# Kernel optimization log

Hardware: AMD Instinct MI355X
Metric: run time of the kernel (lower is better)

Reference implementation:

```python
import jax, jax.numpy as jnp
import numpy as np

B, T, D, H = 4, 2048, 1024, 4
DK = D // H      # head_k_dim = 256
DV = D // H      # head_v_dim = 256
M = DK           # num_slots defaults to head_k_dim
GATE_NORM = 16.0
CLAMP_MIN, CLAMP_MAX = -32.0, 32.0
EPS = 1e-5
ROPE_BASE = 10000.0


def setup_inputs() -> dict:
    key = jax.random.key(0)
    ks = jax.random.split(key, 8)
    sd = 0.02  # stands in for xavier_uniform with gain 2**-2.5
    return {
        "hidden_states": jax.random.normal(ks[0], (B, T, D), jnp.float32),
        "q_w": jax.random.normal(ks[1], (D, D), jnp.float32) * sd,
        "k_w": jax.random.normal(ks[2], (D, D), jnp.float32) * sd,
        "v_w": jax.random.normal(ks[3], (D, D), jnp.float32) * sd,
        "g_w": jax.random.normal(ks[4], (D, D), jnp.float32) * sd,
        "s_w": jax.random.normal(ks[5], (D, H * M), jnp.float32) * sd,
        "sg_w": jax.random.normal(ks[6], (D, H), jnp.float32) * sd,
        "gn_w": jnp.ones((DV,), jnp.float32),
        "o_w": jax.random.normal(ks[7], (D, D), jnp.float32) * sd,
    }


def _rope(x):
    # x: [B, T, H, DK]; non-interleaved (flash-attn style) rotary, full head dim
    half = x.shape[-1] // 2
    inv = 1.0 / (ROPE_BASE ** (jnp.arange(half, dtype=jnp.float32) / half))
    ang = jnp.arange(x.shape[1], dtype=jnp.float32)[:, None] * inv[None, :]  # [T, half]
    cos = jnp.cos(ang)[None, :, None, :]
    sin = jnp.sin(ang)[None, :, None, :]
    x1, x2 = x[..., :half], x[..., half:]
    return jnp.concatenate([x1 * cos - x2 * sin, x2 * cos + x1 * sin], -1)


def _abc(q, k, v, s):
    # ABC linear attention with slot memory (fla chunk_abc semantics, g=None path).
    # q, k: [B,H,T,DK]; v: [B,H,T,DV]; s: [B,H,T,M] (clamped slot logits)
    scale = q.shape[-1] ** -0.5
    z = jax.lax.cumlogsumexp(s, axis=2)                    # running log-normalizer
    s_n = jnp.exp(s - z)                                   # normalized slot write weights
    g = jnp.exp(jnp.concatenate([z[:, :, :1], z[:, :, :-1]], 2) - z)  # per-step decay in (0,1]

    tm = lambda x: jnp.moveaxis(x, 2, 0)                   # time-major for scan

    # stage 1: key memory  hk[B,H,DK,M];  ok_t = scale * q_t @ hk_t
    def step_k(hk, inp):
        q_t, k_t, s_t, g_t = inp
        hk = hk * g_t[:, :, None, :] + k_t[..., None] * s_t[:, :, None, :]
        return hk, jnp.einsum('bhk,bhkm->bhm', q_t, hk)
    hk0 = jnp.zeros(q.shape[:2] + (q.shape[-1], s.shape[-1]), q.dtype)
    _, ok = jax.lax.scan(step_k, hk0, (tm(q * scale), tm(k), tm(s_n), tm(g)))

    qv = jax.nn.softmax(ok, axis=-1)                       # slot read weights, [T,B,H,M]

    # stage 2: value memory  hv[B,H,M,DV];  ov_t = qv_t @ hv_t
    def step_v(hv, inp):
        qv_t, v_t, s_t, g_t = inp
        hv = hv * g_t[..., None] + s_t[..., None] * v_t[:, :, None, :]
        return hv, jnp.einsum('bhm,bhmv->bhv', qv_t, hv)
    hv0 = jnp.zeros(v.shape[:2] + (s.shape[-1], v.shape[-1]), v.dtype)
    _, ov = jax.lax.scan(step_v, hv0, (qv, tm(v), tm(s_n), tm(g)))
    return jnp.moveaxis(ov, 0, 2)                          # [B,H,T,DV]


def reference(hidden_states, q_w, k_w, v_w, g_w, s_w, sg_w, gn_w, o_w):
    x = hidden_states
    q = (x @ q_w).reshape(B, T, H, DK)
    k = (x @ k_w).reshape(B, T, H, DK)
    v = (x @ v_w).reshape(B, T, H, DV).transpose(0, 2, 1, 3)       # [B,H,T,DV]
    q, k = _rope(q), _rope(k)
    q = q.transpose(0, 2, 1, 3)                                    # [B,H,T,DK]
    k = k.transpose(0, 2, 1, 3)

    s = (x @ s_w).reshape(B, T, H, M).transpose(0, 2, 1, 3)        # [B,H,T,M]
    s = jnp.clip(s, CLAMP_MIN, CLAMP_MAX)

    sg = jax.nn.log_sigmoid(x @ sg_w).transpose(0, 2, 1) / GATE_NORM  # [B,H,T]
    k = k * jnp.exp(jnp.cumsum(sg, axis=2))[..., None]

    o = _abc(q, k, v, s).transpose(0, 2, 1, 3)                     # [B,T,H,DV]

    g = (x @ g_w).reshape(B, T, H, DV)
    rms = o * jax.lax.rsqrt(jnp.mean(o * o, axis=-1, keepdims=True) + EPS) * gn_w
    o = (rms * g * jax.nn.sigmoid(g)).reshape(B, T, D)             # RMSNorm + swish gate
    return o @ o_w
```

## Files before the change

kernel.cpp:

```cpp
#include <hip/hip_runtime.h>
#include <hip/hip_bf16.h>
#include <stdint.h>
#include <stddef.h>
#include <math.h>

typedef __bf16 bf8_t __attribute__((ext_vector_type(8)));
typedef __bf16 bf4_t __attribute__((ext_vector_type(4)));
typedef float  f4_t  __attribute__((ext_vector_type(4)));
typedef unsigned int u32;

#define DEV static __device__ __forceinline__

namespace abc {
constexpr int B = 4, T = 2048, D = 1024, H = 4;
constexpr int BT = B * T;
constexpr int CH = 64;
constexpr int NC = T / CH;
constexpr int BH = B * H;
constexpr float SCALE = 0.0625f;
constexpr float GN = 16.0f;
constexpr float EPS = 1e-5f;
}

DEV f4_t mfma16(bf8_t a, bf8_t b, f4_t c) {
  return __builtin_amdgcn_mfma_f32_16x16x32_bf16(a, b, c, 0, 0, 0);
}

DEV void glds16(const void* g, void* l) {
  __builtin_amdgcn_global_load_lds(
      (const __attribute__((address_space(1))) u32*)g,
      (__attribute__((address_space(3))) u32*)l, 16, 0, 0);
}

DEV __bf16* slice_addr(__bf16* base, int row, int cg ) {
  return base + (((cg >> 2) * 2 + (row >> 7)) * 4096
               + ((((row & 127) << 2) | ((cg & 3) ^ (row & 3))) * 8));
}
DEV const __bf16* slice_addr(const __bf16* base, int row, int cg) {
  return base + (((cg >> 2) * 2 + (row >> 7)) * 4096
               + ((((row & 127) << 2) | ((cg & 3) ^ (row & 3))) * 8));
}

DEV void stage_lin(const __bf16* __restrict__ g, __bf16* lds, int tid) {
  #pragma unroll
  for (int i = 0; i < 2; i++)
    glds16(g + (size_t)(i * 256 + tid) * 8, lds + (i * 256 + (tid & ~63)) * 8);
}

template<int ROWS>
DEV void stage(const __bf16* __restrict__ g, int S ,
               __bf16* lds, int tid) {
  #pragma unroll
  for (int i = 0; i < ROWS / 64; i++) {
    int p = i * 256 + tid;
    int m = p >> 2;
    int q = (p & 3) ^ (m & 3);
    glds16(g + (size_t)m * S + q * 8, lds + (i * 256 + (tid & ~63)) * 8);
  }
}
DEV bf8_t bfrag(const __bf16* sl, int m, int quad) {
  return *reinterpret_cast<const bf8_t*>(sl + m * 32 + ((quad ^ (m & 3)) << 3));
}

DEV void ring_pre(int s) {
  if (s < 46)       asm volatile("s_waitcnt vmcnt(4)" ::: "memory");
  else if (s == 46) asm volatile("s_waitcnt vmcnt(2)" ::: "memory");
  else              asm volatile("s_waitcnt vmcnt(0)" ::: "memory");
  asm volatile("s_waitcnt lgkmcnt(0)" ::: "memory");
  asm volatile("s_barrier" ::: "memory");
}

DEV void stage_g(const __bf16* __restrict__ g, int S, __bf16* lds, int tid) {
  int m = tid >> 2;
  int q = (tid & 3) ^ ((m >> 1) & 3);
  glds16(g + (size_t)m * S + q * 8, lds + (tid & ~63) * 8);
}
DEV bf8_t bfrag_g(const __bf16* sl, int m, int quad) {
  return *reinterpret_cast<const bf8_t*>(sl + m * 32 + (((quad ^ (m >> 1)) & 3) << 3));
}

__global__ __launch_bounds__(256)
void cvt_x_kernel(const float* __restrict__ x, __bf16* __restrict__ xb)
{
  const int idx = blockIdx.x * 256 + threadIdx.x;
  const float4* src = reinterpret_cast<const float4*>(x);
  float4 a = src[(size_t)idx * 2];
  float4 b = src[(size_t)idx * 2 + 1];
  bf8_t o;
  o[0] = (__bf16)a.x; o[1] = (__bf16)a.y; o[2] = (__bf16)a.z; o[3] = (__bf16)a.w;
  o[4] = (__bf16)b.x; o[5] = (__bf16)b.y; o[6] = (__bf16)b.z; o[7] = (__bf16)b.w;
  reinterpret_cast<bf8_t*>(xb)[idx] = o;
}

__global__ __launch_bounds__(256)
void cvt_w_kernel(const float* __restrict__ w0, const float* __restrict__ w1,
                  const float* __restrict__ w2, const float* __restrict__ w3,
                  const float* __restrict__ w4, const float* __restrict__ w5,
                  __bf16* __restrict__ wt)
{
  const int z = blockIdx.z;
  const float* W = (z == 0) ? w0 : (z == 1) ? w1 : (z == 2) ? w2
                 : (z == 3) ? w3 : (z == 4) ? w4 : w5;
  const int n0 = blockIdx.x * 64, k0 = blockIdx.y * 64;
  __shared__ __bf16 Ts[64][72];
  const int tid = threadIdx.x;
  #pragma unroll
  for (int i = 0; i < 4; i++) {
    int p = tid + 256 * i;
    int row = p >> 4, c4 = p & 15;
    float4 v = *reinterpret_cast<const float4*>(W + (size_t)(k0 + row) * 1024 + n0 + c4 * 4);
    Ts[c4 * 4 + 0][row] = (__bf16)v.x;
    Ts[c4 * 4 + 1][row] = (__bf16)v.y;
    Ts[c4 * 4 + 2][row] = (__bf16)v.z;
    Ts[c4 * 4 + 3][row] = (__bf16)v.w;
  }
  __syncthreads();
  #pragma unroll
  for (int i = 0; i < 2; i++) {
    int p = tid + 256 * i;
    int n = p >> 3, kq = p & 7;
    bf8_t o = *reinterpret_cast<const bf8_t*>(&Ts[n][kq * 8]);
    *reinterpret_cast<bf8_t*>(wt + (size_t)z * 1024 * 1024 + (size_t)(n0 + n) * 1024 + k0 + kq * 8) = o;
  }
}

template<bool OUT_BF16, int NZ>
__global__ __launch_bounds__(512, 2)
void gemm256_kernel(const __bf16* __restrict__ A, const __bf16* __restrict__ BtB,
                    void* __restrict__ Cp)
{
  using namespace abc;
  constexpr int K = 1024;
  constexpr int NZT = 4 * NZ;
  const int bflat = blockIdx.x;
  const int xcd = bflat & 7;
  const int j = bflat >> 3;
  const int m_local = j / NZT;
  const int nz = j % NZT;
  const int nt = nz & 3, z = nz >> 2;
  const int m0 = (xcd * 4 + m_local) * 256;
  const int n0 = nt * 256;
  const __bf16* Bt = BtB + (size_t)z * K * 1024;

  __shared__ __bf16 LA[2][4][4096];
  __shared__ __bf16 LB[2][4][4096];

  const int tid = threadIdx.x;
  const int lane = tid & 63, wv = tid >> 6;
  const int wr = wv >> 2, wc = wv & 3;
  const int quad = lane >> 4, l16 = lane & 15;
  const f4_t fzero = {0.f, 0.f, 0.f, 0.f};
  f4_t acc[8][4];
  #pragma unroll
  for (int fr = 0; fr < 8; fr++)
    #pragma unroll
    for (int fc = 0; fc < 4; fc++) acc[fr][fc] = fzero;

  auto issue4 = [&](int kt, int ks) {
    const int db = kt & 1;
    const int kcol = kt * 64 + ks * 32;
    stage_g(A  + (size_t)(m0 +   0) * K + kcol, K, &LA[db][0 + ks][0], tid);
    stage_g(A  + (size_t)(m0 + 128) * K + kcol, K, &LA[db][2 + ks][0], tid);
    stage_g(Bt + (size_t)(n0 +   0) * K + kcol, K, &LB[db][0 + ks][0], tid);
    stage_g(Bt + (size_t)(n0 + 128) * K + kcol, K, &LB[db][2 + ks][0], tid);
  };

  issue4(0, 0); issue4(0, 1);

  for (int kt = 0; kt < 16; kt++) {
    const int db = kt & 1;
    const bool last = (kt == 15);
    #pragma unroll
    for (int ks = 0; ks < 2; ks++) {
      if (last && ks == 1) asm volatile("s_waitcnt vmcnt(0)\ns_barrier" ::: "memory");
      else                 asm volatile("s_waitcnt vmcnt(4)\ns_barrier" ::: "memory");
      bf8_t af[8], bfv[4];
      #pragma unroll
      for (int fr = 0; fr < 8; fr++)
        af[fr] = bfrag_g(&LA[db][wr * 2 + ks][0], fr * 16 + l16, quad);
      #pragma unroll
      for (int fc = 0; fc < 4; fc++)
        bfv[fc] = bfrag_g(&LB[db][(wc >> 1) * 2 + ks][0], (wc & 1) * 64 + fc * 16 + l16, quad);
      if (!last) issue4(kt + 1, ks);
      __builtin_amdgcn_s_setprio(1);
      #pragma unroll
      for (int fr = 0; fr < 8; fr++)
        #pragma unroll
        for (int fc = 0; fc < 4; fc++)
          acc[fr][fc] = mfma16(af[fr], bfv[fc], acc[fr][fc]);
      __builtin_amdgcn_s_setprio(0);
    }
  }

  const int crow = m0 + wr * 128, ccol = n0 + wc * 64;
  if (OUT_BF16) {
    __bf16* C = (__bf16*)Cp + (size_t)z * BT * 1024;
    #pragma unroll
    for (int fr = 0; fr < 8; fr++)
      #pragma unroll
      for (int fc = 0; fc < 4; fc++)
        #pragma unroll
        for (int r = 0; r < 4; r++)
          C[(size_t)(crow + fr * 16 + quad * 4 + r) * 1024 + ccol + fc * 16 + l16] =
              (__bf16)acc[fr][fc][r];
  } else {
    float* C = (float*)Cp;
    #pragma unroll
    for (int fr = 0; fr < 8; fr++)
      #pragma unroll
      for (int fc = 0; fc < 4; fc++)
        #pragma unroll
        for (int r = 0; r < 4; r++)
          C[(size_t)(crow + fr * 16 + quad * 4 + r) * 1024 + ccol + fc * 16 + l16] =
              acc[fr][fc][r];
  }
}

__global__ __launch_bounds__(256)
void sg_kernel(const float* __restrict__ x, const float* __restrict__ sgw,
               float* __restrict__ sgl)
{
  using namespace abc;
  const int wvid = threadIdx.x >> 6, lane = threadIdx.x & 63;
  const int bt = blockIdx.x * 4 + wvid;
  const float* xr = x + (size_t)bt * 1024;
  float a0 = 0, a1 = 0, a2 = 0, a3 = 0;
  #pragma unroll 4
  for (int u = 0; u < 16; u++) {
    int i = u * 64 + lane;
    float xv = xr[i];
    float4 w = *reinterpret_cast<const float4*>(sgw + (size_t)i * 4);
    a0 += xv * w.x; a1 += xv * w.y; a2 += xv * w.z; a3 += xv * w.w;
  }
  #pragma unroll
  for (int off = 32; off > 0; off >>= 1) {
    a0 += __shfl_down(a0, off);
    a1 += __shfl_down(a1, off);
    a2 += __shfl_down(a2, off);
    a3 += __shfl_down(a3, off);
  }
  if (lane == 0) {
    const int b = bt >> 11, t = bt & (T - 1);
    float r[4] = {a0, a1, a2, a3};
    #pragma unroll
    for (int h = 0; h < 4; h++) {
      float v = r[h];
      float ls = fminf(v, 0.f) - log1pf(expf(-fabsf(v)));
      sgl[(size_t)(b * 4 + h) * T + t] = ls * (1.0f / GN);
    }
  }
}

__global__ __launch_bounds__(256)
void scan_kernel(const float* __restrict__ sgl, float* __restrict__ sgc)
{
  using namespace abc;
  const int bh = blockIdx.x;
  const float* in = sgl + (size_t)bh * T;
  float* out = sgc + (size_t)bh * T;
  __shared__ float part[256];
  const int tid = threadIdx.x;
  float v[8]; float s = 0.f;
  #pragma unroll
  for (int i = 0; i < 8; i++) { v[i] = in[tid * 8 + i]; s += v[i]; }
  part[tid] = s;
  __syncthreads();
  for (int off = 1; off < 256; off <<= 1) {
    float a = (tid >= off) ? part[tid - off] : 0.f;
    __syncthreads();
    part[tid] += a;
    __syncthreads();
  }
  float run = (tid > 0) ? part[tid - 1] : 0.f;
  #pragma unroll
  for (int i = 0; i < 8; i++) { run += v[i]; out[tid * 8 + i] = run; }
}

__global__ __launch_bounds__(256)
void prep_kernel(__bf16* __restrict__ q, __bf16* __restrict__ k,
                 __bf16* __restrict__ s, const float* __restrict__ sgc)
{
  using namespace abc;
  const int bt = blockIdx.x;
  const int b = bt >> 11, t = bt & (T - 1);
  const int tid = threadIdx.x;
  const size_t ro = (size_t)bt * 1024;
  #pragma unroll
  for (int i = 0; i < 2; i++) {
    int p = tid + 256 * i;
    int h = p >> 7, d = p & 127;
    float inv = expf(-(float)d * (9.210340371976184f / 128.0f));
    float ang = (float)t * inv;
    float sn, cs;
    sincosf(ang, &sn, &cs);
    size_t base = ro + (size_t)h * 256 + d;
    float q1 = (float)q[base], q2 = (float)q[base + 128];
    q[base]       = (__bf16)(q1 * cs - q2 * sn);
    q[base + 128] = (__bf16)(q2 * cs + q1 * sn);
    float dec = expf(sgc[(size_t)(b * 4 + h) * T + t]);
    float k1 = (float)k[base], k2 = (float)k[base + 128];
    k[base]       = (__bf16)((k1 * cs - k2 * sn) * dec);
    k[base + 128] = (__bf16)((k2 * cs + k1 * sn) * dec);
  }
  #pragma unroll
  for (int i = 0; i < 4; i++) {
    int e = tid + 256 * i;
    float v = (float)s[ro + e];
    v = fminf(fmaxf(v, -32.f), 32.f);
    s[ro + e] = (__bf16)expf(v);
  }
}

template<bool NEW0, bool NEW1>
__global__ __launch_bounds__(256)
void transpose_kernel(const __bf16* __restrict__ s0, const __bf16* __restrict__ s1,
                      __bf16* __restrict__ d0, __bf16* __restrict__ d1)
{
  using namespace abc;
  const int c = blockIdx.x, bh = blockIdx.y, z = blockIdx.z;
  const int b = bh >> 2, h = bh & 3;
  const size_t R = (size_t)b * T + (size_t)c * CH;
  const int F = h * 256;
  const __bf16* src = z ? s1 : s0;
  __bf16* dst = (z ? d1 : d0) + ((size_t)bh * NC + c) * (256 * 64);
  const bool NEWL = z ? NEW1 : NEW0;
  __shared__ __bf16 L[256 * 64];
  const int tid = threadIdx.x;
  #pragma unroll
  for (int j = 0; j < 8; j++) {
    int p = tid + 256 * j;
    int t = p >> 5, fc = p & 31;
    bf8_t v = *reinterpret_cast<const bf8_t*>(src + (R + t) * 1024 + F + fc * 8);
    const int sw = ((t >> 3) ^ (fc & 7)) * 8 + (t & 7);
    #pragma unroll
    for (int u = 0; u < 8; u++)
      L[(fc * 8 + u) * 64 + sw] = v[u];
  }
  __syncthreads();
  #pragma unroll
  for (int j = 0; j < 8; j++) {
    int p = tid + 256 * j;
    int f = p >> 3, q = p & 7;
    int phys = q ^ ((f >> 3) & 7);
    bf8_t o = *reinterpret_cast<const bf8_t*>(&L[f * 64 + phys * 8]);
    __bf16* daddr = NEWL ? slice_addr(dst, f, q)
                         : dst + (size_t)f * 64 + q * 8;
    *reinterpret_cast<bf8_t*>(daddr) = o;
  }
}

__global__ __launch_bounds__(256)
void chunkstate_kernel(const __bf16* __restrict__ KT, const __bf16* __restrict__ VT,
                       const __bf16* __restrict__ AT,
                       __bf16* __restrict__ HKc, __bf16* __restrict__ HVc,
                       float* __restrict__ csA)
{
  using namespace abc;
  const int c = blockIdx.x, bh = blockIdx.y, part = blockIdx.z;
  const size_t TB = ((size_t)bh * NC + c) * (256 * 64);
  const bool isHV = part >= 2;
  const int p2 = part & 1;
  const __bf16* Aop = (isHV ? VT : AT) + TB;
  const __bf16* Bop = (isHV ? AT : KT) + TB;
  const int tid = threadIdx.x;
  if (part == 2) {
    float ssum = 0.f;
    #pragma unroll
    for (int u = 0; u < 8; u++) {
      bf8_t v = *reinterpret_cast<const bf8_t*>(slice_addr(AT + TB, tid, u));
      #pragma unroll
      for (int w = 0; w < 8; w++) ssum += (float)v[w];
    }
    csA[((size_t)bh * NC + c) * 256 + tid] = ssum;
  }
  const int lane = tid & 63, wvid = tid >> 6;
  const int quad = lane >> 4, l16 = lane & 15;
  const int row0 = p2 * 128 + wvid * 32;
  const f4_t fzero = {0.f, 0.f, 0.f, 0.f};
  f4_t acc[2][16];
  #pragma unroll
  for (int a = 0; a < 2; a++)
    #pragma unroll
    for (int ct = 0; ct < 16; ct++) acc[a][ct] = fzero;
  #pragma unroll
  for (int ks = 0; ks < 2; ks++) {
    const int cg = ks * 4 + quad;
    bf8_t af0 = *reinterpret_cast<const bf8_t*>(slice_addr(Aop, row0 + l16, cg));
    bf8_t af1 = *reinterpret_cast<const bf8_t*>(slice_addr(Aop, row0 + 16 + l16, cg));
    #pragma unroll
    for (int ct = 0; ct < 16; ct++) {
      bf8_t bv;
      if (isHV)
        bv = *reinterpret_cast<const bf8_t*>(slice_addr(Bop, ct * 16 + l16, cg));
      else
        bv = *reinterpret_cast<const bf8_t*>(Bop + (size_t)(ct * 16 + l16) * 64 + ks * 32 + quad * 8);
      acc[0][ct] = mfma16(af0, bv, acc[0][ct]);
      acc[1][ct] = mfma16(af1, bv, acc[1][ct]);
    }
  }
  __bf16* out = (isHV ? HVc : HKc) + ((size_t)bh * NC + c) * 65536;
  #pragma unroll
  for (int rt = 0; rt < 2; rt++)
    #pragma unroll
    for (int ct = 0; ct < 16; ct++)
      #pragma unroll
      for (int r = 0; r < 4; r++) {
        const int mg = row0 + rt * 16 + quad * 4 + r;
        const int n  = ct * 16 + l16;
        *(slice_addr(out, mg, n >> 3) + (n & 7)) = (__bf16)acc[rt][ct][r];
      }
}

__global__ __launch_bounds__(256)
void prefix_state_kernel(__bf16* __restrict__ HKc, __bf16* __restrict__ HVc)
{
  using namespace abc;
  const int bh = blockIdx.y;
  __bf16* base = (blockIdx.z ? HVc : HKc) + (size_t)bh * NC * 65536;
  const int e = (blockIdx.x * 256 + threadIdx.x) * 8;
  float run[8];
  #pragma unroll
  for (int u = 0; u < 8; u++) run[u] = 0.f;
  #pragma unroll 4
  for (int c = 0; c < NC; c++) {
    __bf16* p = base + (size_t)c * 65536 + e;
    bf8_t v = *reinterpret_cast<const bf8_t*>(p);
    bf8_t o;
    #pragma unroll
    for (int u = 0; u < 8; u++) { o[u] = (__bf16)run[u]; run[u] += (float)v[u]; }
    *reinterpret_cast<bf8_t*>(p) = o;
  }
}

__global__ __launch_bounds__(256)
void prefix_csa_kernel(float* __restrict__ csA)
{
  using namespace abc;
  const int bh = blockIdx.x, m = threadIdx.x;
  float run = 0.f;
  for (int c = 0; c < NC; c++) {
    float* p = csA + ((size_t)bh * NC + c) * 256 + m;
    float v = *p; *p = run; run += v;
  }
}

__global__ __launch_bounds__(256)
void attn_kernel(const __bf16* __restrict__ qg, const __bf16* __restrict__ kg,
                 const __bf16* __restrict__ ag, const __bf16* __restrict__ gg,
                 const __bf16* __restrict__ ATp, const __bf16* __restrict__ VTp,
                 const __bf16* __restrict__ HKp, const __bf16* __restrict__ HVp,
                 const float* __restrict__ Zp, const float* __restrict__ gnw,
                 __bf16* __restrict__ yout)
{
  using namespace abc;
  const int c = blockIdx.x, bh = blockIdx.y;
  const int b = bh >> 2, h = bh & 3;
  const size_t R = (size_t)b * T + (size_t)c * CH;
  const int F = h * 256;
  const int tid = threadIdx.x;
  const int lane = tid & 63, wvid = tid >> 6;
  const int quad = lane >> 4, l16 = lane & 15;

  __shared__ __bf16 ST[4][4096];
  __shared__ __bf16 Ws[64][264];
  __shared__ __bf16 S1s[64][72];
  __shared__ float zs[256];
  __shared__ float gns[256];

  const __bf16* atb = ATp + ((size_t)bh * NC + c) * (256 * 64);
  const __bf16* vtb = VTp + ((size_t)bh * NC + c) * (256 * 64);
  const __bf16* hkb = HKp + ((size_t)bh * NC + c) * 65536;
  const __bf16* hvb = HVp + ((size_t)bh * NC + c) * 65536;
  const __bf16* kbase = kg + R * 1024 + F;
  const __bf16* abase = ag + R * 1024 + F;

  zs[tid] = Zp[((size_t)bh * NC + c) * 256 + tid];
  gns[tid] = gnw[tid];
  __syncthreads();

  const __bf16* qrow = qg + (R + wvid * 16 + l16) * 1024 + F;
  bf8_t aq[8];
  #pragma unroll
  for (int ks = 0; ks < 8; ks++)
    aq[ks] = *reinterpret_cast<const bf8_t*>(qrow + ks * 32 + quad * 8);

  const f4_t fzero = {0.f, 0.f, 0.f, 0.f};

  auto issue = [&](int s) {
    if (s >= 48) return;
    __bf16* buf = &ST[s & 3][0];
    if (s < 4) {
      stage<64>(kbase + (2 * s) * 32, 1024, buf, tid);
      stage<64>(kbase + (2 * s + 1) * 32, 1024, buf + 2048, tid);
    } else if (s < 8) {
      stage_lin(atb + (s - 4) * 4096, buf, tid);
    } else if (s < 24) {
      stage_lin(hkb + (s - 8) * 4096, buf, tid);
    } else if (s < 28) {
      int j = s - 24;
      stage<64>(abase + (2 * j) * 32, 1024, buf, tid);
      stage<64>(abase + (2 * j + 1) * 32, 1024, buf + 2048, tid);
    } else if (s < 44) {
      stage_lin(hvb + (s - 28) * 4096, buf, tid);
    } else {
      stage_lin(vtb + (s - 44) * 4096, buf, tid);
    }
  };

  issue(0); issue(1); issue(2);

  f4_t s1a[4];
  #pragma unroll
  for (int it = 0; it < 4; it++) s1a[it] = fzero;
  #pragma unroll
  for (int j = 0; j < 4; j++) {
    ring_pre(j);
    issue(j + 3);
    const __bf16* sl = &ST[j & 3][0];
    #pragma unroll
    for (int ks2 = 0; ks2 < 2; ks2++) {
      bf8_t a = aq[2 * j + ks2];
      const __bf16* sb = sl + ks2 * 2048;
      #pragma unroll
      for (int it = 0; it < 4; it++)
        s1a[it] = mfma16(a, bfrag(sb, it * 16 + l16, quad), s1a[it]);
    }
  }
  #pragma unroll
  for (int it = 0; it < 4; it++)
    #pragma unroll
    for (int r = 0; r < 4; r++) {
      int tl = wvid * 16 + quad * 4 + r;
      int il = it * 16 + l16;
      S1s[tl][il] = (il <= tl) ? (__bf16)s1a[it][r] : (__bf16)0.0f;
    }

  f4_t aok[16], acum[16];
  #pragma unroll
  for (int mt = 0; mt < 16; mt++) { aok[mt] = fzero; acum[mt] = fzero; }
  #pragma unroll
  for (int j = 0; j < 4; j++) {
    int s = 4 + j, iks = j >> 1, rh = j & 1;
    ring_pre(s);
    issue(s + 3);
    const __bf16* sl = &ST[s & 3][0];
    bf8_t s1f = *reinterpret_cast<const bf8_t*>(&S1s[wvid * 16 + l16][iks * 32 + quad * 8]);
    bf8_t lf;
    #pragma unroll
    for (int u = 0; u < 8; u++)
      lf[u] = (iks * 32 + quad * 8 + u <= wvid * 16 + l16) ? (__bf16)1.0f : (__bf16)0.0f;
    #pragma unroll
    for (int m8 = 0; m8 < 8; m8++) {
      bf8_t bfa = bfrag(sl, m8 * 16 + l16, quad);
      aok[rh * 8 + m8]  = mfma16(s1f, bfa, aok[rh * 8 + m8]);
      acum[rh * 8 + m8] = mfma16(lf,  bfa, acum[rh * 8 + m8]);
    }
  }

  #pragma unroll
  for (int j = 0; j < 16; j++) {
    int s = 8 + j, ks = j >> 1, rh = j & 1;
    ring_pre(s);
    issue(s + 3);
    const __bf16* sl = &ST[s & 3][0];
    #pragma unroll
    for (int m8 = 0; m8 < 8; m8++) {
      bf8_t bv = bfrag(sl, m8 * 16 + l16, quad);
      aok[rh * 8 + m8] = mfma16(aq[ks], bv, aok[rh * 8 + m8]);
    }
  }

  #pragma unroll
  for (int r = 0; r < 4; r++) {
    float ovv[16], sa[16];
    float mx = -3.0e38f;
    #pragma unroll
    for (int mt = 0; mt < 16; mt++) {
      sa[mt] = zs[mt * 16 + l16] + acum[mt][r];
      ovv[mt] = SCALE * aok[mt][r] / sa[mt];
      mx = fmaxf(mx, ovv[mt]);
    }
    #pragma unroll
    for (int off = 1; off < 16; off <<= 1) mx = fmaxf(mx, __shfl_xor(mx, off));
    float se = 0.f;
    #pragma unroll
    for (int mt = 0; mt < 16; mt++) { ovv[mt] = __expf(ovv[mt] - mx); se += ovv[mt]; }
    #pragma unroll
    for (int off = 1; off < 16; off <<= 1) se += __shfl_xor(se, off);
    float inv = 1.0f / se;
    int tl = wvid * 16 + quad * 4 + r;
    #pragma unroll
    for (int mt = 0; mt < 16; mt++)
      Ws[tl][mt * 16 + l16] = (__bf16)(ovv[mt] * inv / sa[mt]);
  }

  f4_t pacc[4];
  #pragma unroll
  for (int it = 0; it < 4; it++) pacc[it] = fzero;
  #pragma unroll
  for (int j = 0; j < 4; j++) {
    int s = 24 + j;
    ring_pre(s);
    issue(s + 3);
    const __bf16* sl = &ST[s & 3][0];
    #pragma unroll
    for (int ks2 = 0; ks2 < 2; ks2++) {
      int ks = 2 * j + ks2;
      bf8_t wf = *reinterpret_cast<const bf8_t*>(&Ws[wvid * 16 + l16][ks * 32 + quad * 8]);
      const __bf16* sb = sl + ks2 * 2048;
      #pragma unroll
      for (int it = 0; it < 4; it++)
        pacc[it] = mfma16(wf, bfrag(sb, it * 16 + l16, quad), pacc[it]);
    }
  }
  #pragma unroll
  for (int it = 0; it < 4; it++)
    #pragma unroll
    for (int r = 0; r < 4; r++) {
      int tl = wvid * 16 + quad * 4 + r;
      int il = it * 16 + l16;
      S1s[tl][il] = (il <= tl) ? (__bf16)pacc[it][r] : (__bf16)0.0f;
    }

  f4_t oacc[16];
  #pragma unroll
  for (int vt = 0; vt < 16; vt++) oacc[vt] = fzero;
  #pragma unroll
  for (int j = 0; j < 16; j++) {
    int s = 28 + j, ks = j >> 1, rh = j & 1;
    ring_pre(s);
    issue(s + 3);
    const __bf16* sl = &ST[s & 3][0];
    bf8_t wf = *reinterpret_cast<const bf8_t*>(&Ws[wvid * 16 + l16][ks * 32 + quad * 8]);
    #pragma unroll
    for (int v8 = 0; v8 < 8; v8++) {
      bf8_t bv = bfrag(sl, v8 * 16 + l16, quad);
      oacc[rh * 8 + v8] = mfma16(wf, bv, oacc[rh * 8 + v8]);
    }
  }

  #pragma unroll
  for (int j = 0; j < 4; j++) {
    int s = 44 + j, iks = j >> 1, rh = j & 1;
    ring_pre(s);
    issue(s + 3);
    const __bf16* sl = &ST[s & 3][0];
    bf8_t pf = *reinterpret_cast<const bf8_t*>(&S1s[wvid * 16 + l16][iks * 32 + quad * 8]);
    #pragma unroll
    for (int v8 = 0; v8 < 8; v8++) {
      bf8_t bvt = bfrag(sl, v8 * 16 + l16, quad);
      oacc[rh * 8 + v8] = mfma16(pf, bvt, oacc[rh * 8 + v8]);
    }
  }

  #pragma unroll
  for (int r = 0; r < 4; r++) {
    float ss = 0.f;
    #pragma unroll
    for (int vt = 0; vt < 16; vt++) ss += oacc[vt][r] * oacc[vt][r];
    #pragma unroll
    for (int off = 1; off < 16; off <<= 1) ss += __shfl_xor(ss, off);
    float rinv = rsqrtf(ss * (1.0f / 256.0f) + EPS);
    int tl = wvid * 16 + quad * 4 + r;
    const __bf16* grow = gg + (R + tl) * 1024 + F;
    __bf16* yrow = yout + (R + tl) * 1024 + F;
    #pragma unroll
    for (int vt = 0; vt < 16; vt++) {
      int v = vt * 16 + l16;
      float gvl = (float)grow[v];
      float yv = oacc[vt][r] * rinv * gns[v] * gvl / (1.0f + __expf(-gvl));
      yrow[v] = (__bf16)yv;
    }
  }
}

extern "C" void kernel_launch(void* const* d_in, const int* in_sizes, int n_in,
                              void* d_out, int out_size, void* d_ws, size_t ws_size,
                              hipStream_t stream) {
  using namespace abc;
  (void)in_sizes; (void)n_in; (void)out_size; (void)ws_size;
  const float* x    = (const float*)d_in[0];
  const float* q_w  = (const float*)d_in[1];
  const float* k_w  = (const float*)d_in[2];
  const float* v_w  = (const float*)d_in[3];
  const float* g_w  = (const float*)d_in[4];
  const float* s_w  = (const float*)d_in[5];
  const float* sg_w = (const float*)d_in[6];
  const float* gn_w = (const float*)d_in[7];
  const float* o_w  = (const float*)d_in[8];
  float* out = (float*)d_out;

  char* ws = (char*)d_ws;
  const size_t PROJ = (size_t)BT * 1024;
  __bf16* proj = (__bf16*)ws;
  __bf16* q_bf = proj + 0 * PROJ;
  __bf16* k_bf = proj + 1 * PROJ;
  __bf16* v_bf = proj + 2 * PROJ;
  __bf16* g_bf = proj + 3 * PROJ;
  __bf16* a_bf = proj + 4 * PROJ;
  __bf16* xb   = proj + 5 * PROJ;
  float* sgl = (float*)(ws + (size_t)96 * 1024 * 1024);
  float* sgc = sgl + (size_t)BH * T;
  float* csA = sgc + (size_t)BH * T;
  __bf16* HKc = (__bf16*)(ws + (size_t)97 * 1024 * 1024);
  __bf16* HVc = HKc + (size_t)BH * NC * 65536;
  __bf16* wt  = (__bf16*)(ws + (size_t)225 * 1024 * 1024);
  __bf16* KT  = (__bf16*)(ws + (size_t)237 * 1024 * 1024);
  __bf16* VT  = xb;
  __bf16* AT  = v_bf;
  __bf16* y_bf = KT;

  dim3 blk(256);
  dim3 blk512(512);
  cvt_w_kernel<<<dim3(16, 16, 6), blk, 0, stream>>>(q_w, k_w, v_w, g_w, s_w, o_w, wt);
  cvt_x_kernel<<<dim3(BT * 1024 / (256 * 8)), blk, 0, stream>>>(x, xb);
  gemm256_kernel<true, 5><<<dim3(32 * 4 * 5), blk512, 0, stream>>>(xb, wt, proj);
  sg_kernel<<<dim3(BT / 4), blk, 0, stream>>>(x, sg_w, sgl);
  scan_kernel<<<dim3(BH), blk, 0, stream>>>(sgl, sgc);
  prep_kernel<<<dim3(BT), blk, 0, stream>>>(q_bf, k_bf, a_bf, sgc);
  transpose_kernel<false, true><<<dim3(NC, BH, 2), blk, 0, stream>>>(k_bf, v_bf, KT, VT);
  transpose_kernel<true, true><<<dim3(NC, BH, 1), blk, 0, stream>>>(a_bf, a_bf, AT, AT);
  chunkstate_kernel<<<dim3(NC, BH, 4), blk, 0, stream>>>(KT, VT, AT, HKc, HVc, csA);
  prefix_state_kernel<<<dim3(32, BH, 2), blk, 0, stream>>>(HKc, HVc);
  prefix_csa_kernel<<<dim3(BH), blk, 0, stream>>>(csA);
  attn_kernel<<<dim3(NC, BH), blk, 0, stream>>>(
      q_bf, k_bf, a_bf, g_bf, AT, VT, HKc, HVc, csA, gn_w, y_bf);
  gemm256_kernel<false, 1><<<dim3(32 * 4), blk512, 0, stream>>>(
      y_bf, wt + (size_t)5 * 1024 * 1024, out);
}
```

Baseline: 515.9 us.

## Load attention operands directly from global memory instead of LDS ring pipeline

Removes the 4-slot LDS staging ring, with its async global-to-LDS copies, waitcnt and barrier calls, from the attention kernel. MFMA B-fragments for K, A, AT, HK, HV and VT now come straight from global memory into registers, using the precomputed swizzled layout offsets. This drops the per-stage barriers and frees 32KB of LDS, which may raise occupancy. In exchange, each of the four waves now fetches the same operand data separately from global/L2, and the explicit prefetch overlap is lost.

Result: faster. 473.9 us (-8.2%).

```diff
diff --git a/kernel.cpp b/kernel.cpp
--- a/kernel.cpp
+++ b/kernel.cpp
@@ -5,7 +5,6 @@
 #include <math.h>
 
 typedef __bf16 bf8_t __attribute__((ext_vector_type(8)));
-typedef __bf16 bf4_t __attribute__((ext_vector_type(4)));
 typedef float  f4_t  __attribute__((ext_vector_type(4)));
 typedef unsigned int u32;
 
@@ -39,35 +38,6 @@
 DEV const __bf16* slice_addr(const __bf16* base, int row, int cg) {
   return base + (((cg >> 2) * 2 + (row >> 7)) * 4096
                + ((((row & 127) << 2) | ((cg & 3) ^ (row & 3))) * 8));
-}
-
-DEV void stage_lin(const __bf16* __restrict__ g, __bf16* lds, int tid) {
-  #pragma unroll
-  for (int i = 0; i < 2; i++)
-    glds16(g + (size_t)(i * 256 + tid) * 8, lds + (i * 256 + (tid & ~63)) * 8);
-}
-
-template<int ROWS>
-DEV void stage(const __bf16* __restrict__ g, int S ,
-               __bf16* lds, int tid) {
-  #pragma unroll
-  for (int i = 0; i < ROWS / 64; i++) {
-    int p = i * 256 + tid;
-    int m = p >> 2;
-    int q = (p & 3) ^ (m & 3);
-    glds16(g + (size_t)m * S + q * 8, lds + (i * 256 + (tid & ~63)) * 8);
-  }
-}
-DEV bf8_t bfrag(const __bf16* sl, int m, int quad) {
-  return *reinterpret_cast<const bf8_t*>(sl + m * 32 + ((quad ^ (m & 3)) << 3));
-}
-
-DEV void ring_pre(int s) {
-  if (s < 46)       asm volatile("s_waitcnt vmcnt(4)" ::: "memory");
-  else if (s == 46) asm volatile("s_waitcnt vmcnt(2)" ::: "memory");
-  else              asm volatile("s_waitcnt vmcnt(0)" ::: "memory");
-  asm volatile("s_waitcnt lgkmcnt(0)" ::: "memory");
-  asm volatile("s_barrier" ::: "memory");
 }
 
 DEV void stage_g(const __bf16* __restrict__ g, int S, __bf16* lds, int tid) {
@@ -461,7 +431,6 @@
   const int lane = tid & 63, wvid = tid >> 6;
   const int quad = lane >> 4, l16 = lane & 15;
 
-  __shared__ __bf16 ST[4][4096];
   __shared__ __bf16 Ws[64][264];
   __shared__ __bf16 S1s[64][72];
   __shared__ float zs[256];
@@ -478,6 +447,9 @@
   gns[tid] = gnw[tid];
   __syncthreads();
 
+  const int lsw = l16 * 32 + ((quad ^ (l16 & 3)) << 3);
+  const int rowoff = l16 * 1024 + quad * 8;
+
   const __bf16* qrow = qg + (R + wvid * 16 + l16) * 1024 + F;
   bf8_t aq[8];
   #pragma unroll
@@ -486,44 +458,15 @@
 
   const f4_t fzero = {0.f, 0.f, 0.f, 0.f};
 
-  auto issue = [&](int s) {
-    if (s >= 48) return;
-    __bf16* buf = &ST[s & 3][0];
-    if (s < 4) {
-      stage<64>(kbase + (2 * s) * 32, 1024, buf, tid);
-      stage<64>(kbase + (2 * s + 1) * 32, 1024, buf + 2048, tid);
-    } else if (s < 8) {
-      stage_lin(atb + (s - 4) * 4096, buf, tid);
-    } else if (s < 24) {
-      stage_lin(hkb + (s - 8) * 4096, buf, tid);
-    } else if (s < 28) {
-      int j = s - 24;
-      stage<64>(abase + (2 * j) * 32, 1024, buf, tid);
-      stage<64>(abase + (2 * j + 1) * 32, 1024, buf + 2048, tid);
-    } else if (s < 44) {
-      stage_lin(hvb + (s - 28) * 4096, buf, tid);
-    } else {
-      stage_lin(vtb + (s - 44) * 4096, buf, tid);
-    }
-  };
-
-  issue(0); issue(1); issue(2);
-
   f4_t s1a[4];
   #pragma unroll
   for (int it = 0; it < 4; it++) s1a[it] = fzero;
   #pragma unroll
-  for (int j = 0; j < 4; j++) {
-    ring_pre(j);
-    issue(j + 3);
-    const __bf16* sl = &ST[j & 3][0];
-    #pragma unroll
-    for (int ks2 = 0; ks2 < 2; ks2++) {
-      bf8_t a = aq[2 * j + ks2];
-      const __bf16* sb = sl + ks2 * 2048;
-      #pragma unroll
-      for (int it = 0; it < 4; it++)
-        s1a[it] = mfma16(a, bfrag(sb, it * 16 + l16, quad), s1a[it]);
+  for (int ks = 0; ks < 8; ks++) {
+    #pragma unroll
+    for (int it = 0; it < 4; it++) {
+      bf8_t bk = *reinterpret_cast<const bf8_t*>(kbase + it * 16 * 1024 + rowoff + ks * 32);
+      s1a[it] = mfma16(aq[ks], bk, s1a[it]);
     }
   }
   #pragma unroll
@@ -539,34 +482,32 @@
   #pragma unroll
   for (int mt = 0; mt < 16; mt++) { aok[mt] = fzero; acum[mt] = fzero; }
   #pragma unroll
-  for (int j = 0; j < 4; j++) {
-    int s = 4 + j, iks = j >> 1, rh = j & 1;
-    ring_pre(s);
-    issue(s + 3);
-    const __bf16* sl = &ST[s & 3][0];
+  for (int iks = 0; iks < 2; iks++) {
     bf8_t s1f = *reinterpret_cast<const bf8_t*>(&S1s[wvid * 16 + l16][iks * 32 + quad * 8]);
     bf8_t lf;
     #pragma unroll
     for (int u = 0; u < 8; u++)
       lf[u] = (iks * 32 + quad * 8 + u <= wvid * 16 + l16) ? (__bf16)1.0f : (__bf16)0.0f;
     #pragma unroll
-    for (int m8 = 0; m8 < 8; m8++) {
-      bf8_t bfa = bfrag(sl, m8 * 16 + l16, quad);
-      aok[rh * 8 + m8]  = mfma16(s1f, bfa, aok[rh * 8 + m8]);
-      acum[rh * 8 + m8] = mfma16(lf,  bfa, acum[rh * 8 + m8]);
-    }
-  }
-
-  #pragma unroll
-  for (int j = 0; j < 16; j++) {
-    int s = 8 + j, ks = j >> 1, rh = j & 1;
-    ring_pre(s);
-    issue(s + 3);
-    const __bf16* sl = &ST[s & 3][0];
-    #pragma unroll
-    for (int m8 = 0; m8 < 8; m8++) {
-      bf8_t bv = bfrag(sl, m8 * 16 + l16, quad);
-      aok[rh * 8 + m8] = mfma16(aq[ks], bv, aok[rh * 8 + m8]);
+    for (int rh = 0; rh < 2; rh++) {
+      #pragma unroll
+      for (int m8 = 0; m8 < 8; m8++) {
+        bf8_t bfa = *reinterpret_cast<const bf8_t*>(atb + (iks * 2 + rh) * 4096 + m8 * 512 + lsw);
+        aok[rh * 8 + m8]  = mfma16(s1f, bfa, aok[rh * 8 + m8]);
+        acum[rh * 8 + m8] = mfma16(lf,  bfa, acum[rh * 8 + m8]);
+      }
+    }
+  }
+
+  #pragma unroll
+  for (int ks = 0; ks < 8; ks++) {
+    #pragma unroll
+    for (int rh = 0; rh < 2; rh++) {
+      #pragma unroll
+      for (int m8 = 0; m8 < 8; m8++) {
+        bf8_t bv = *reinterpret_cast<const bf8_t*>(hkb + (ks * 2 + rh) * 4096 + m8 * 512 + lsw);
+        aok[rh * 8 + m8] = mfma16(aq[ks], bv, aok[rh * 8 + m8]);
+      }
     }
   }
 
@@ -598,19 +539,12 @@
   #pragma unroll
   for (int it = 0; it < 4; it++) pacc[it] = fzero;
   #pragma unroll
-  for (int j = 0; j < 4; j++) {
-    int s = 24 + j;
-    ring_pre(s);
-    issue(s + 3);
-    const __bf16* sl = &ST[s & 3][0];
-    #pragma unroll
-    for (int ks2 = 0; ks2 < 2; ks2++) {
-      int ks = 2 * j + ks2;
-      bf8_t wf = *reinterpret_cast<const bf8_t*>(&Ws[wvid * 16 + l16][ks * 32 + quad * 8]);
-      const __bf16* sb = sl + ks2 * 2048;
-      #pragma unroll
-      for (int it = 0; it < 4; it++)
-        pacc[it] = mfma16(wf, bfrag(sb, it * 16 + l16, quad), pacc[it]);
+  for (int ks = 0; ks < 8; ks++) {
+    bf8_t wf = *reinterpret_cast<const bf8_t*>(&Ws[wvid * 16 + l16][ks * 32 + quad * 8]);
+    #pragma unroll
+    for (int it = 0; it < 4; it++) {
+      bf8_t ba = *reinterpret_cast<const bf8_t*>(abase + it * 16 * 1024 + rowoff + ks * 32);
+      pacc[it] = mfma16(wf, ba, pacc[it]);
     }
   }
   #pragma unroll
@@ -626,30 +560,28 @@
   #pragma unroll
   for (int vt = 0; vt < 16; vt++) oacc[vt] = fzero;
   #pragma unroll
-  for (int j = 0; j < 16; j++) {
-    int s = 28 + j, ks = j >> 1, rh = j & 1;
-    ring_pre(s);
-    issue(s + 3);
-    const __bf16* sl = &ST[s & 3][0];
+  for (int ks = 0; ks < 8; ks++) {
     bf8_t wf = *reinterpret_cast<const bf8_t*>(&Ws[wvid * 16 + l16][ks * 32 + quad * 8]);
     #pragma unroll
-    for (int v8 = 0; v8 < 8; v8++) {
-      bf8_t bv = bfrag(sl, v8 * 16 + l16, quad);
-      oacc[rh * 8 + v8] = mfma16(wf, bv, oacc[rh * 8 + v8]);
-    }
-  }
-
-  #pragma unroll
-  for (int j = 0; j < 4; j++) {
-    int s = 44 + j, iks = j >> 1, rh = j & 1;
-    ring_pre(s);
-    issue(s + 3);
-    const __bf16* sl = &ST[s & 3][0];
+    for (int rh = 0; rh < 2; rh++) {
+      #pragma unroll
+      for (int v8 = 0; v8 < 8; v8++) {
+        bf8_t bv = *reinterpret_cast<const bf8_t*>(hvb + (ks * 2 + rh) * 4096 + v8 * 512 + lsw);
+        oacc[rh * 8 + v8] = mfma16(wf, bv, oacc[rh * 8 + v8]);
+      }
+    }
+  }
+
+  #pragma unroll
+  for (int iks = 0; iks < 2; iks++) {
     bf8_t pf = *reinterpret_cast<const bf8_t*>(&S1s[wvid * 16 + l16][iks * 32 + quad * 8]);
     #pragma unroll
-    for (int v8 = 0; v8 < 8; v8++) {
-      bf8_t bvt = bfrag(sl, v8 * 16 + l16, quad);
-      oacc[rh * 8 + v8] = mfma16(pf, bvt, oacc[rh * 8 + v8]);
+    for (int rh = 0; rh < 2; rh++) {
+      #pragma unroll
+      for (int v8 = 0; v8 < 8; v8++) {
+        bf8_t bvt = *reinterpret_cast<const bf8_t*>(vtb + (iks * 2 + rh) * 4096 + v8 * 512 + lsw);
+        oacc[rh * 8 + v8] = mfma16(pf, bvt, oacc[rh * 8 + v8]);
+      }
     }
   }
 
```
